# Kernel tuning notes

Hardware: AMD Instinct MI355X
Metric: run time of the kernel (lower is better)

Reference implementation:

```python
import jax, jax.numpy as jnp
import numpy as np

STEPS = 8  # number of scaling-and-squaring steps


def _identity_grid(D, H, W, dtype):
    # (D, H, W, 3) voxel-coordinate identity transformation
    z = jnp.arange(D, dtype=dtype)
    y = jnp.arange(H, dtype=dtype)
    x = jnp.arange(W, dtype=dtype)
    return jnp.stack(jnp.meshgrid(z, y, x, indexing='ij'), axis=-1)


def _pull_wrap(v, phi):
    """Trilinear sampling of field v at voxel coords phi with circular ('dft') bound.

    v:   (B, D, H, W, 3) vector field (values)
    phi: (B, D, H, W, 3) sampling coordinates in voxel space (z, y, x order)
    """
    B, D, H, W, C = v.shape
    f = jnp.floor(phi)
    w1 = phi - f          # weight of the +1 corner
    w0 = 1.0 - w1
    i0 = f.astype(jnp.int32)
    dims = jnp.array([D, H, W], dtype=jnp.int32)
    i0 = jnp.mod(i0, dims)          # wrap (dft) boundary
    i1 = jnp.mod(i0 + 1, dims)
    zs, ys, xs = (i0[..., 0], i1[..., 0]), (i0[..., 1], i1[..., 1]), (i0[..., 2], i1[..., 2])
    wzs, wys, wxs = (w0[..., 0], w1[..., 0]), (w0[..., 1], w1[..., 1]), (w0[..., 2], w1[..., 2])
    vflat = v.reshape(B, D * H * W, C)
    out = jnp.zeros_like(v)
    for a in range(2):
        for b in range(2):
            for c in range(2):
                lin = (zs[a] * H + ys[b]) * W + xs[c]              # (B, D, H, W)
                vals = jnp.take_along_axis(vflat, lin.reshape(B, -1, 1), axis=1)
                vals = vals.reshape(B, D, H, W, C)
                out = out + (wzs[a] * wys[b] * wxs[c])[..., None] * vals
    return out


def setup_inputs() -> dict:
    key = jax.random.key(0)
    velocity = jax.random.normal(key, (2, 128, 128, 128, 3), dtype=jnp.float32)
    return {"velocity": velocity}


def reference(velocity):
    # Scaling and squaring: v <- v/2^K; repeat K times: v <- v + v o (id + v)
    B, D, H, W, C = velocity.shape
    grid = _identity_grid(D, H, W, velocity.dtype)[None]  # (1, D, H, W, 3)
    v = velocity / (2.0 ** STEPS)
    for _ in range(STEPS):
        v = v + _pull_wrap(v, grid + v)
    # displacement=False -> return transformation field id + displacement
    return grid + v
```

## Files before the change

### kernel.cpp

```cpp
#include <hip/hip_runtime.h>
#include <hip/hip_fp16.h>


#define DHW   (128 * 128 * 128)
#define NVOX  (2 * DHW)
#define RW    129

__device__ __forceinline__ __half2 bc_h2(unsigned u) {
    return *reinterpret_cast<__half2*>(&u);
}

__device__ __forceinline__ void acc_cell(uint2 c, float w,
                                         float& az, float& ay, float& ax) {
    __half2 c0 = bc_h2(c.x), c1 = bc_h2(c.y);
    az = fmaf(w, __low2float(c0),  az);
    ay = fmaf(w, __high2float(c0), ay);
    ax = fmaf(w, __low2float(c1),  ax);
}

template <bool IN_F32, int H, int BX, int BZ>
__global__ __launch_bounds__(512) void sq_stencil(
    const float* __restrict__ vel,
    const uint2* __restrict__ fin,
    uint2* __restrict__ fout)
{
    constexpr int LBX = (BX == 64) ? 6 : 5;
    constexpr int LBZ = (BZ == 8) ? 3 : 2;
    constexpr int TX = BX + 2 * H, TY = 8 + 2 * H, TZ = BZ + 2 * H;
    constexpr int TS = TX * TY * TZ;
    constexpr int ZT  = 512 >> (LBX + 3);
    constexpr int VPT = BZ / ZT;
    constexpr int NXB = 128 / BX, LNX = 7 - LBX;
    constexpr int NZB = 128 / BZ, LNZ = 7 - LBZ;
    static_assert(TS * 8 <= 64 * 1024, "tile exceeds 64KB static LDS");
    static_assert(VPT == 4, "geometry expects 4 voxels/thread");
    __shared__ uint2 tile[TS];

    int t = (int)threadIdx.x;
    int b = (int)blockIdx.x;
    int X = (b & (NXB - 1)) << LBX;
    int b2 = b >> LNX;
    int Y = (b2 & 15) << 3;
    int b3 = b2 >> 4;
    int Z = (b3 & (NZB - 1)) << LBZ;
    int batch = b3 >> LNZ;
    int bbr = batch << 14;

    for (int idx = t; idx < TS; idx += 512) {
        int xx = idx % TX;
        int rem = idx / TX;
        int yy = rem % TY;
        int zz = rem / TY;
        int gx = (X - H + xx) & 127;
        int gy = (Y - H + yy) & 127;
        int gz = (Z - H + zz) & 127;
        uint2 c;
        if (IN_F32) {
            const float s = 1.0f / 256.0f;
            size_t a = (size_t)((batch << 21) | (gz << 14) | (gy << 7) | gx) * 3;
            __half2 p0 = __floats2half2_rn(vel[a] * s, vel[a + 1] * s);
            __half2 p1 = __floats2half2_rn(vel[a + 2] * s, 0.0f);
            c.x = *reinterpret_cast<unsigned*>(&p0);
            c.y = *reinterpret_cast<unsigned*>(&p1);
        } else {
            int rr = bbr + (gz << 7) + gy;
            c = fin[(rr << 7) + rr + gx];
        }
        tile[idx] = c;
    }
    __syncthreads();

    int lx = t & (BX - 1);
    int ly = (t >> LBX) & 7;
    int lz0 = (t >> (LBX + 3)) * VPT;

#pragma unroll
    for (int i = 0; i < VPT; ++i) {
        int lz = lz0 + i;
        int cidx = ((lz + H) * TY + (ly + H)) * TX + (lx + H);
        uint2 c = tile[cidx];
        __half2 c0 = bc_h2(c.x), c1 = bc_h2(c.y);
        float vz = __low2float(c0), vy = __high2float(c0), vx = __low2float(c1);

        float zf = (float)(Z + lz), yf = (float)(Y + ly), xf = (float)(X + lx);
        float pz = zf + vz, py = yf + vy, px = xf + vx;
        float fz = floorf(pz), fy = floorf(py), fx = floorf(px);
        float wz1 = pz - fz, wy1 = py - fy, wx1 = px - fx;
        float wz0 = 1.0f - wz1, wy0 = 1.0f - wy1, wx0 = 1.0f - wx1;

        int izl = (int)fz - Z + H;
        int iyl = (int)fy - Y + H;
        int ixl = (int)fx - X + H;

        float wzy00 = wz0 * wy0, wzy01 = wz0 * wy1;
        float wzy10 = wz1 * wy0, wzy11 = wz1 * wy1;

        float az = 0.0f, ay = 0.0f, ax = 0.0f;
        int i00 = (izl * TY + iyl) * TX + ixl;
        int i01 = i00 + TX;
        int i10 = i00 + TY * TX;
        int i11 = i10 + TX;

        acc_cell(tile[i00],     wzy00 * wx0, az, ay, ax);
        acc_cell(tile[i00 + 1], wzy00 * wx1, az, ay, ax);
        acc_cell(tile[i01],     wzy01 * wx0, az, ay, ax);
        acc_cell(tile[i01 + 1], wzy01 * wx1, az, ay, ax);
        acc_cell(tile[i10],     wzy10 * wx0, az, ay, ax);
        acc_cell(tile[i10 + 1], wzy10 * wx1, az, ay, ax);
        acc_cell(tile[i11],     wzy11 * wx0, az, ay, ax);
        acc_cell(tile[i11 + 1], wzy11 * wx1, az, ay, ax);

        float oz = vz + az, oy = vy + ay, ox = vx + ax;

        __half2 p0 = __floats2half2_rn(oz, oy);
        __half2 p1 = __floats2half2_rn(ox, 0.0f);
        uint2 sd;
        sd.x = *reinterpret_cast<unsigned*>(&p0);
        sd.y = *reinterpret_cast<unsigned*>(&p1);
        int z_ = Z + lz, y_ = Y + ly, x_ = X + lx;
        int rS = bbr + (z_ << 7) + y_;
        int pidx = (rS << 7) + rS + x_;
        fout[pidx] = sd;
        if (x_ == 0) fout[pidx + 128] = sd;
    }
}

__device__ __forceinline__ void acc_pair(uint4 g, float wl, float wr,
                                         float& az, float& ay, float& ax) {
    __half2 h0 = bc_h2(g.x);
    __half2 h1 = bc_h2(g.y);
    __half2 h2 = bc_h2(g.z);
    __half2 h3 = bc_h2(g.w);
    az += wl * __low2float(h0)  + wr * __low2float(h2);
    ay += wl * __high2float(h0) + wr * __high2float(h2);
    ax += wl * __low2float(h1)  + wr * __low2float(h3);
}

template <bool IN_F32, bool OUT_F32>
__global__ __launch_bounds__(1024) void sq_step_p(
    const void* __restrict__ vin_, void* __restrict__ vout_)
{
    const float* vinf = (const float*)vin_;
    const uint2* vinh = (const uint2*)vin_;

    int t = (int)threadIdx.x;
    int b = (int)blockIdx.x;
    int x = ((b & 1) << 6) | (t & 63);
    int y = (((b >> 1) & 31) << 2) | ((t >> 6) & 3);
    int z = (((b >> 6) & 31) << 2) | (t >> 8);
    int batch = b >> 11;

    const float s = IN_F32 ? (1.0f / 256.0f) : 1.0f;

    int bbr = batch << 14;
    int r   = bbr + (z << 7) + y;

    float vz, vy, vx;
    if (IN_F32) {
        size_t base = ((size_t)(batch << 21) + (z << 14) + (y << 7) + x) * 3;
        vz = vinf[base + 0] * s;
        vy = vinf[base + 1] * s;
        vx = vinf[base + 2] * s;
    } else {
        uint2 c = vinh[(r << 7) + r + x];
        __half2 c0 = bc_h2(c.x), c1 = bc_h2(c.y);
        vz = __low2float(c0); vy = __high2float(c0); vx = __low2float(c1);
    }

    float pz = (float)z + vz, py = (float)y + vy, px = (float)x + vx;
    float fz = floorf(pz), fy = floorf(py), fx = floorf(px);
    float wz1 = pz - fz, wy1 = py - fy, wx1 = px - fx;
    float wz0 = 1.0f - wz1, wy0 = 1.0f - wy1, wx0 = 1.0f - wx1;

    int iz0 = ((int)fz) & 127, iy0 = ((int)fy) & 127, ix0 = ((int)fx) & 127;
    int iz1 = (iz0 + 1) & 127, iy1 = (iy0 + 1) & 127;

    float wzy00 = wz0 * wy0, wzy01 = wz0 * wy1;
    float wzy10 = wz1 * wy0, wzy11 = wz1 * wy1;

    float az = 0.0f, ay = 0.0f, ax = 0.0f;

    if (IN_F32) {
        int bb  = batch << 21;
        int ix1 = (ix0 + 1) & 127;
        int zo0 = bb + (iz0 << 14), zo1 = bb + (iz1 << 14);
        int yo0 = iy0 << 7, yo1 = iy1 << 7;
#define CORNER(ZO, YO, IX, WW)                                          \
        {                                                               \
            size_t a = (size_t)((ZO) + (YO) + (IX)) * 3;                \
            float w = (WW);                                             \
            az += w * (vinf[a] * s);                                    \
            ay += w * (vinf[a + 1] * s);                                \
            ax += w * (vinf[a + 2] * s);                                \
        }
        CORNER(zo0, yo0, ix0, wzy00 * wx0)
        CORNER(zo0, yo0, ix1, wzy00 * wx1)
        CORNER(zo0, yo1, ix0, wzy01 * wx0)
        CORNER(zo0, yo1, ix1, wzy01 * wx1)
        CORNER(zo1, yo0, ix0, wzy10 * wx0)
        CORNER(zo1, yo0, ix1, wzy10 * wx1)
        CORNER(zo1, yo1, ix0, wzy11 * wx0)
        CORNER(zo1, yo1, ix1, wzy11 * wx1)
#undef CORNER
    } else {
        int r00 = bbr + (iz0 << 7) + iy0;
        int r01 = bbr + (iz0 << 7) + iy1;
        int r10 = bbr + (iz1 << 7) + iy0;
        int r11 = bbr + (iz1 << 7) + iy1;
        uint4 g00 = *(const uint4*)(vinh + (r00 << 7) + r00 + ix0);
        uint4 g01 = *(const uint4*)(vinh + (r01 << 7) + r01 + ix0);
        uint4 g10 = *(const uint4*)(vinh + (r10 << 7) + r10 + ix0);
        uint4 g11 = *(const uint4*)(vinh + (r11 << 7) + r11 + ix0);
        acc_pair(g00, wzy00 * wx0, wzy00 * wx1, az, ay, ax);
        acc_pair(g01, wzy01 * wx0, wzy01 * wx1, az, ay, ax);
        acc_pair(g10, wzy10 * wx0, wzy10 * wx1, az, ay, ax);
        acc_pair(g11, wzy11 * wx0, wzy11 * wx1, az, ay, ax);
    }

    float oz = vz + az;
    float oy = vy + ay;
    float ox = vx + ax;

    if (OUT_F32) {
        float* voutf = (float*)vout_;
        size_t base = ((size_t)(batch << 21) + (z << 14) + (y << 7) + x) * 3;
        voutf[base + 0] = oz + (float)z;
        voutf[base + 1] = oy + (float)y;
        voutf[base + 2] = ox + (float)x;
    } else {
        __half2 p0 = __floats2half2_rn(oz, oy);
        __half2 p1 = __floats2half2_rn(ox, 0.0f);
        uint2 sd;
        sd.x = *reinterpret_cast<unsigned*>(&p0);
        sd.y = *reinterpret_cast<unsigned*>(&p1);
        uint2* vouth = (uint2*)vout_;
        int pidx = (r << 7) + r + x;
        vouth[pidx] = sd;
        if (x == 0) vouth[pidx + 128] = sd;
    }
}

extern "C" void kernel_launch(void* const* d_in, const int* in_sizes, int n_in,
                              void* d_out, int out_size, void* d_ws, size_t ws_size,
                              hipStream_t stream) {
    const float* vel = (const float*)d_in[0];
    float* out = (float*)d_out;

    const size_t PB = (size_t)2 * 128 * 128 * RW * 8;

    dim3 sblock(512);
    dim3 sgrid(2048);
    dim3 ggrid(NVOX / 1024), gblock(1024);

    if (ws_size >= 2 * PB) {
        uint2* P0 = (uint2*)d_ws;
        uint2* P1 = (uint2*)((char*)d_ws + PB);

        sq_stencil<true,  1, 64, 4><<<sgrid, sblock, 0, stream>>>(vel, nullptr, P0);
        sq_stencil<false, 1, 64, 4><<<sgrid, sblock, 0, stream>>>(nullptr, P0, P1);
        sq_stencil<false, 1, 64, 4><<<sgrid, sblock, 0, stream>>>(nullptr, P1, P0);
        sq_stencil<false, 1, 64, 4><<<sgrid, sblock, 0, stream>>>(nullptr, P0, P1);
        sq_stencil<false, 1, 64, 4><<<sgrid, sblock, 0, stream>>>(nullptr, P1, P0);
        sq_stencil<false, 1, 64, 4><<<sgrid, sblock, 0, stream>>>(nullptr, P0, P1);
        sq_stencil<false, 2, 32, 8><<<sgrid, sblock, 0, stream>>>(nullptr, P1, P0);
        sq_step_p<false, true ><<<ggrid, gblock, 0, stream>>>(P0, out);
    } else {
        void* ws = d_ws;
        sq_step_p<true,  false><<<ggrid, gblock, 0, stream>>>(vel, ws);
        sq_step_p<false, false><<<ggrid, gblock, 0, stream>>>(ws,  out);
        sq_step_p<false, false><<<ggrid, gblock, 0, stream>>>(out, ws);
        sq_step_p<false, false><<<ggrid, gblock, 0, stream>>>(ws,  out);
        sq_step_p<false, false><<<ggrid, gblock, 0, stream>>>(out, ws);
        sq_step_p<false, false><<<ggrid, gblock, 0, stream>>>(ws,  out);
        sq_step_p<false, false><<<ggrid, gblock, 0, stream>>>(out, ws);
        sq_step_p<false, true ><<<ggrid, gblock, 0, stream>>>(ws,  out);
    }
}
```

Before: 280.7 us.

## Pipeline stencil steps over z-slabs with double-buffered LDS and separate f32 conversion

Each stencil block now walks four consecutive z-slabs, prefetching the next slab's halo into registers while computing the current one, then writing it into a second LDS buffer. The fp32-to-fp16 scaling moves into a dedicated vectorized conversion kernel, and intermediate steps use an unpadded layout, with only the last stencil writing the padded layout for the final gather kernel. This aims to hide global load latency and cut redundant halo traffic, at the cost of fewer blocks, more registers, one extra launch and a larger workspace requirement.

```diff
diff --git a/kernel.cpp b/kernel.cpp
--- a/kernel.cpp
+++ b/kernel.cpp
@@ -18,23 +18,40 @@
     ax = fmaf(w, __low2float(c1),  ax);
 }
 
-template <bool IN_F32, int H, int BX, int BZ>
-__global__ __launch_bounds__(512) void sq_stencil(
-    const float* __restrict__ vel,
-    const uint2* __restrict__ fin,
-    uint2* __restrict__ fout)
+__global__ __launch_bounds__(512) void conv_f32_f16(
+    const float* __restrict__ vel, uint2* __restrict__ out)
+{
+    int i = (((int)blockIdx.x << 9) | (int)threadIdx.x) << 1;
+    size_t a = (size_t)i * 3;
+    const float s = 1.0f / 256.0f;
+    float2 l0 = *(const float2*)(vel + a);
+    float2 l1 = *(const float2*)(vel + a + 2);
+    float2 l2 = *(const float2*)(vel + a + 4);
+    __half2 a0 = __floats2half2_rn(l0.x * s, l0.y * s);
+    __half2 a1 = __floats2half2_rn(l1.x * s, 0.0f);
+    __half2 b0 = __floats2half2_rn(l1.y * s, l2.x * s);
+    __half2 b1 = __floats2half2_rn(l2.y * s, 0.0f);
+    uint4 o;
+    o.x = *reinterpret_cast<unsigned*>(&a0);
+    o.y = *reinterpret_cast<unsigned*>(&a1);
+    o.z = *reinterpret_cast<unsigned*>(&b0);
+    o.w = *reinterpret_cast<unsigned*>(&b1);
+    *(uint4*)(out + i) = o;
+}
+
+template <int H, int BX, int BZ, int NB, bool PAD_OUT>
+__global__ __launch_bounds__(512) void sq_sten_pipe(
+    const uint2* __restrict__ fin, uint2* __restrict__ fout)
 {
     constexpr int LBX = (BX == 64) ? 6 : 5;
-    constexpr int LBZ = (BZ == 8) ? 3 : 2;
     constexpr int TX = BX + 2 * H, TY = 8 + 2 * H, TZ = BZ + 2 * H;
     constexpr int TS = TX * TY * TZ;
-    constexpr int ZT  = 512 >> (LBX + 3);
-    constexpr int VPT = BZ / ZT;
+    constexpr int PF = (TS + 511) / 512;
+    constexpr int VPT = (BX * BZ) / 64;
     constexpr int NXB = 128 / BX, LNX = 7 - LBX;
-    constexpr int NZB = 128 / BZ, LNZ = 7 - LBZ;
-    static_assert(TS * 8 <= 64 * 1024, "tile exceeds 64KB static LDS");
-    static_assert(VPT == 4, "geometry expects 4 voxels/thread");
-    __shared__ uint2 tile[TS];
+    static_assert(2 * TS * 8 <= 64 * 1024, "dbuf exceeds 64KB static LDS");
+    static_assert(128 % (BZ * NB) == 0 && 128 / (BZ * NB) == 8, "z grouping");
+    __shared__ uint2 lds[2][TS];
 
     int t = (int)threadIdx.x;
     int b = (int)blockIdx.x;
@@ -42,87 +59,119 @@
     int b2 = b >> LNX;
     int Y = (b2 & 15) << 3;
     int b3 = b2 >> 4;
-    int Z = (b3 & (NZB - 1)) << LBZ;
-    int batch = b3 >> LNZ;
-    int bbr = batch << 14;
-
-    for (int idx = t; idx < TS; idx += 512) {
-        int xx = idx % TX;
-        int rem = idx / TX;
-        int yy = rem % TY;
-        int zz = rem / TY;
-        int gx = (X - H + xx) & 127;
-        int gy = (Y - H + yy) & 127;
-        int gz = (Z - H + zz) & 127;
-        uint2 c;
-        if (IN_F32) {
-            const float s = 1.0f / 256.0f;
-            size_t a = (size_t)((batch << 21) | (gz << 14) | (gy << 7) | gx) * 3;
-            __half2 p0 = __floats2half2_rn(vel[a] * s, vel[a + 1] * s);
-            __half2 p1 = __floats2half2_rn(vel[a + 2] * s, 0.0f);
-            c.x = *reinterpret_cast<unsigned*>(&p0);
-            c.y = *reinterpret_cast<unsigned*>(&p1);
-        } else {
-            int rr = bbr + (gz << 7) + gy;
-            c = fin[(rr << 7) + rr + gx];
+    int Z0 = (b3 & 7) * (BZ * NB);
+    int batch = b3 >> 3;
+    int bb21 = batch << 21;
+
+    int soff[PF], szz[PF];
+#pragma unroll
+    for (int p = 0; p < PF; ++p) {
+        int idx = t + p * 512;
+        if (idx < TS) {
+            int xx = idx % TX;
+            int rem = idx / TX;
+            int yy = rem % TY;
+            int zz = rem / TY;
+            int gx = (X - H + xx) & 127;
+            int gy = (Y - H + yy) & 127;
+            soff[p] = (gy << 7) | gx;
+            szz[p] = zz;
         }
-        tile[idx] = c;
-    }
+    }
+
+    uint2 R[PF];
+#define STAGE_LOAD(ZB)                                                  \
+    _Pragma("unroll")                                                   \
+    for (int p = 0; p < PF; ++p) {                                      \
+        int idx = t + p * 512;                                          \
+        if (idx < TS) {                                                 \
+            int gz = ((ZB) - H + szz[p]) & 127;                         \
+            R[p] = fin[bb21 + (gz << 14) + soff[p]];                    \
+        }                                                               \
+    }
+#define DS_WRITE(BUF)                                                   \
+    _Pragma("unroll")                                                   \
+    for (int p = 0; p < PF; ++p) {                                      \
+        int idx = t + p * 512;                                          \
+        if (idx < TS) (BUF)[idx] = R[p];                                \
+    }
+
+    STAGE_LOAD(Z0)
+    DS_WRITE(lds[0])
     __syncthreads();
 
     int lx = t & (BX - 1);
     int ly = (t >> LBX) & 7;
     int lz0 = (t >> (LBX + 3)) * VPT;
 
+    for (int i = 0; i < NB; ++i) {
+        int Z = Z0 + i * BZ;
+        const uint2* tile = lds[i & 1];
+        if (i + 1 < NB) { STAGE_LOAD(Z0 + (i + 1) * BZ) }
+
+        uint2 sd[VPT];
 #pragma unroll
-    for (int i = 0; i < VPT; ++i) {
-        int lz = lz0 + i;
-        int cidx = ((lz + H) * TY + (ly + H)) * TX + (lx + H);
-        uint2 c = tile[cidx];
-        __half2 c0 = bc_h2(c.x), c1 = bc_h2(c.y);
-        float vz = __low2float(c0), vy = __high2float(c0), vx = __low2float(c1);
-
-        float zf = (float)(Z + lz), yf = (float)(Y + ly), xf = (float)(X + lx);
-        float pz = zf + vz, py = yf + vy, px = xf + vx;
-        float fz = floorf(pz), fy = floorf(py), fx = floorf(px);
-        float wz1 = pz - fz, wy1 = py - fy, wx1 = px - fx;
-        float wz0 = 1.0f - wz1, wy0 = 1.0f - wy1, wx0 = 1.0f - wx1;
-
-        int izl = (int)fz - Z + H;
-        int iyl = (int)fy - Y + H;
-        int ixl = (int)fx - X + H;
-
-        float wzy00 = wz0 * wy0, wzy01 = wz0 * wy1;
-        float wzy10 = wz1 * wy0, wzy11 = wz1 * wy1;
-
-        float az = 0.0f, ay = 0.0f, ax = 0.0f;
-        int i00 = (izl * TY + iyl) * TX + ixl;
-        int i01 = i00 + TX;
-        int i10 = i00 + TY * TX;
-        int i11 = i10 + TX;
-
-        acc_cell(tile[i00],     wzy00 * wx0, az, ay, ax);
-        acc_cell(tile[i00 + 1], wzy00 * wx1, az, ay, ax);
-        acc_cell(tile[i01],     wzy01 * wx0, az, ay, ax);
-        acc_cell(tile[i01 + 1], wzy01 * wx1, az, ay, ax);
-        acc_cell(tile[i10],     wzy10 * wx0, az, ay, ax);
-        acc_cell(tile[i10 + 1], wzy10 * wx1, az, ay, ax);
-        acc_cell(tile[i11],     wzy11 * wx0, az, ay, ax);
-        acc_cell(tile[i11 + 1], wzy11 * wx1, az, ay, ax);
-
-        float oz = vz + az, oy = vy + ay, ox = vx + ax;
-
-        __half2 p0 = __floats2half2_rn(oz, oy);
-        __half2 p1 = __floats2half2_rn(ox, 0.0f);
-        uint2 sd;
-        sd.x = *reinterpret_cast<unsigned*>(&p0);
-        sd.y = *reinterpret_cast<unsigned*>(&p1);
-        int z_ = Z + lz, y_ = Y + ly, x_ = X + lx;
-        int rS = bbr + (z_ << 7) + y_;
-        int pidx = (rS << 7) + rS + x_;
-        fout[pidx] = sd;
-        if (x_ == 0) fout[pidx + 128] = sd;
-    }
+        for (int v = 0; v < VPT; ++v) {
+            int lz = lz0 + v;
+            int cidx = ((lz + H) * TY + (ly + H)) * TX + (lx + H);
+            uint2 c = tile[cidx];
+            __half2 c0 = bc_h2(c.x), c1 = bc_h2(c.y);
+            float vz = __low2float(c0), vy = __high2float(c0), vx = __low2float(c1);
+
+            float pz = (float)(Z + lz) + vz;
+            float py = (float)(Y + ly) + vy;
+            float px = (float)(X + lx) + vx;
+            float fz = floorf(pz), fy = floorf(py), fx = floorf(px);
+            float wz1 = pz - fz, wy1 = py - fy, wx1 = px - fx;
+            float wz0 = 1.0f - wz1, wy0 = 1.0f - wy1, wx0 = 1.0f - wx1;
+
+            int izl = (int)fz - Z + H;
+            int iyl = (int)fy - Y + H;
+            int ixl = (int)fx - X + H;
+
+            float wzy00 = wz0 * wy0, wzy01 = wz0 * wy1;
+            float wzy10 = wz1 * wy0, wzy11 = wz1 * wy1;
+
+            float az = 0.0f, ay = 0.0f, ax = 0.0f;
+            int i00 = (izl * TY + iyl) * TX + ixl;
+            int i01 = i00 + TX;
+            int i10 = i00 + TY * TX;
+            int i11 = i10 + TX;
+
+            acc_cell(tile[i00],     wzy00 * wx0, az, ay, ax);
+            acc_cell(tile[i00 + 1], wzy00 * wx1, az, ay, ax);
+            acc_cell(tile[i01],     wzy01 * wx0, az, ay, ax);
+            acc_cell(tile[i01 + 1], wzy01 * wx1, az, ay, ax);
+            acc_cell(tile[i10],     wzy10 * wx0, az, ay, ax);
+            acc_cell(tile[i10 + 1], wzy10 * wx1, az, ay, ax);
+            acc_cell(tile[i11],     wzy11 * wx0, az, ay, ax);
+            acc_cell(tile[i11 + 1], wzy11 * wx1, az, ay, ax);
+
+            __half2 p0 = __floats2half2_rn(vz + az, vy + ay);
+            __half2 p1 = __floats2half2_rn(vx + ax, 0.0f);
+            sd[v].x = *reinterpret_cast<unsigned*>(&p0);
+            sd[v].y = *reinterpret_cast<unsigned*>(&p1);
+        }
+
+        if (i + 1 < NB) { DS_WRITE(lds[(i + 1) & 1]) }
+
+#pragma unroll
+        for (int v = 0; v < VPT; ++v) {
+            int lz = lz0 + v;
+            int z_ = Z + lz, y_ = Y + ly, x_ = X + lx;
+            if (PAD_OUT) {
+                int rS = (batch << 14) + (z_ << 7) + y_;
+                int pidx = (rS << 7) + rS + x_;
+                fout[pidx] = sd[v];
+                if (x_ == 0) fout[pidx + 128] = sd[v];
+            } else {
+                fout[bb21 | (z_ << 14) | (y_ << 7) | x_] = sd[v];
+            }
+        }
+        __syncthreads();
+    }
+#undef STAGE_LOAD
+#undef DS_WRITE
 }
 
 __device__ __forceinline__ void acc_pair(uint4 g, float wl, float wr,
@@ -246,24 +295,28 @@
     const float* vel = (const float*)d_in[0];
     float* out = (float*)d_out;
 
+    const size_t UB = (size_t)NVOX * 8;
     const size_t PB = (size_t)2 * 128 * 128 * RW * 8;
 
-    dim3 sblock(512);
-    dim3 sgrid(2048);
+    dim3 cgrid(NVOX / 1024), cblock(512);
+    dim3 pgrid1(512),  pblock(512);
+    dim3 pgrid2(1024);
     dim3 ggrid(NVOX / 1024), gblock(1024);
 
-    if (ws_size >= 2 * PB) {
-        uint2* P0 = (uint2*)d_ws;
-        uint2* P1 = (uint2*)((char*)d_ws + PB);
-
-        sq_stencil<true,  1, 64, 4><<<sgrid, sblock, 0, stream>>>(vel, nullptr, P0);
-        sq_stencil<false, 1, 64, 4><<<sgrid, sblock, 0, stream>>>(nullptr, P0, P1);
-        sq_stencil<false, 1, 64, 4><<<sgrid, sblock, 0, stream>>>(nullptr, P1, P0);
-        sq_stencil<false, 1, 64, 4><<<sgrid, sblock, 0, stream>>>(nullptr, P0, P1);
-        sq_stencil<false, 1, 64, 4><<<sgrid, sblock, 0, stream>>>(nullptr, P1, P0);
-        sq_stencil<false, 1, 64, 4><<<sgrid, sblock, 0, stream>>>(nullptr, P0, P1);
-        sq_stencil<false, 2, 32, 8><<<sgrid, sblock, 0, stream>>>(nullptr, P1, P0);
-        sq_step_p<false, true ><<<ggrid, gblock, 0, stream>>>(P0, out);
+    if (ws_size >= 2 * UB + PB) {
+        uint2* U0 = (uint2*)d_ws;
+        uint2* U1 = (uint2*)((char*)d_ws + UB);
+        uint2* P  = (uint2*)((char*)d_ws + 2 * UB);
+
+        conv_f32_f16<<<cgrid, cblock, 0, stream>>>(vel, U0);
+        sq_sten_pipe<1, 64, 4, 4, false><<<pgrid1, pblock, 0, stream>>>(U0, U1);
+        sq_sten_pipe<1, 64, 4, 4, false><<<pgrid1, pblock, 0, stream>>>(U1, U0);
+        sq_sten_pipe<1, 64, 4, 4, false><<<pgrid1, pblock, 0, stream>>>(U0, U1);
+        sq_sten_pipe<1, 64, 4, 4, false><<<pgrid1, pblock, 0, stream>>>(U1, U0);
+        sq_sten_pipe<1, 64, 4, 4, false><<<pgrid1, pblock, 0, stream>>>(U0, U1);
+        sq_sten_pipe<1, 64, 4, 4, false><<<pgrid1, pblock, 0, stream>>>(U1, U0);
+        sq_sten_pipe<2, 32, 4, 4, true ><<<pgrid2, pblock, 0, stream>>>(U0, P);
+        sq_step_p<false, true ><<<ggrid, gblock, 0, stream>>>(P, out);
     } else {
         void* ws = d_ws;
         sq_step_p<true,  false><<<ggrid, gblock, 0, stream>>>(vel, ws);
```

After: 295.4 us. +5.3%, slower.

## Warp-specialize stencil kernel with double-buffered LDS tiles across z-slabs

Applied to the files above, without the earlier changes.

Each stencil block now processes a 16-deep z range as four 4-slab chunks. Half the threads stage the next halo tile into a second LDS buffer while the other half compute the current chunk. Intermediate fields move to an unpadded layout, and only the last stencil writes the padded layout used by the final gather kernel. This aims to hide global load latency behind compute and cut redundant halo reloads. The cost is that only 256 threads compute per phase, LDS use doubles, and the grid is smaller, which lowers occupancy and parallelism.

```diff
diff --git a/kernel.cpp b/kernel.cpp
--- a/kernel.cpp
+++ b/kernel.cpp
@@ -18,23 +18,65 @@
     ax = fmaf(w, __low2float(c1),  ax);
 }
 
-template <bool IN_F32, int H, int BX, int BZ>
-__global__ __launch_bounds__(512) void sq_stencil(
-    const float* __restrict__ vel,
+template <int TXt, int TYt>
+__device__ __forceinline__ uint2 step_point(const uint2* __restrict__ tile,
+                                            uint2 c, int gz, int gy, int gx,
+                                            int OZ, int OY, int OX)
+{
+    __half2 c0 = bc_h2(c.x), c1 = bc_h2(c.y);
+    float vz = __low2float(c0), vy = __high2float(c0), vx = __low2float(c1);
+
+    float pz = (float)gz + vz, py = (float)gy + vy, px = (float)gx + vx;
+    float fz = floorf(pz), fy = floorf(py), fx = floorf(px);
+    float wz1 = pz - fz, wy1 = py - fy, wx1 = px - fx;
+    float wz0 = 1.0f - wz1, wy0 = 1.0f - wy1, wx0 = 1.0f - wx1;
+
+    int izl = (int)fz - OZ;
+    int iyl = (int)fy - OY;
+    int ixl = (int)fx - OX;
+
+    float wzy00 = wz0 * wy0, wzy01 = wz0 * wy1;
+    float wzy10 = wz1 * wy0, wzy11 = wz1 * wy1;
+
+    float az = 0.0f, ay = 0.0f, ax = 0.0f;
+    int i00 = (izl * TYt + iyl) * TXt + ixl;
+    int i01 = i00 + TXt;
+    int i10 = i00 + TYt * TXt;
+    int i11 = i10 + TXt;
+
+    acc_cell(tile[i00],     wzy00 * wx0, az, ay, ax);
+    acc_cell(tile[i00 + 1], wzy00 * wx1, az, ay, ax);
+    acc_cell(tile[i01],     wzy01 * wx0, az, ay, ax);
+    acc_cell(tile[i01 + 1], wzy01 * wx1, az, ay, ax);
+    acc_cell(tile[i10],     wzy10 * wx0, az, ay, ax);
+    acc_cell(tile[i10 + 1], wzy10 * wx1, az, ay, ax);
+    acc_cell(tile[i11],     wzy11 * wx0, az, ay, ax);
+    acc_cell(tile[i11 + 1], wzy11 * wx1, az, ay, ax);
+
+    __half2 p0 = __floats2half2_rn(vz + az, vy + ay);
+    __half2 p1 = __floats2half2_rn(vx + ax, 0.0f);
+    uint2 sd;
+    sd.x = *reinterpret_cast<unsigned*>(&p0);
+    sd.y = *reinterpret_cast<unsigned*>(&p1);
+    return sd;
+}
+
+template <bool IN_F32, int H, int BX, bool PAD_OUT>
+__global__ __launch_bounds__(512) void sq_sten_ws(
+    const float* __restrict__ velf,
     const uint2* __restrict__ fin,
     uint2* __restrict__ fout)
 {
     constexpr int LBX = (BX == 64) ? 6 : 5;
-    constexpr int LBZ = (BZ == 8) ? 3 : 2;
+    constexpr int BZ = 4, NB = 4;
     constexpr int TX = BX + 2 * H, TY = 8 + 2 * H, TZ = BZ + 2 * H;
     constexpr int TS = TX * TY * TZ;
-    constexpr int ZT  = 512 >> (LBX + 3);
-    constexpr int VPT = BZ / ZT;
     constexpr int NXB = 128 / BX, LNX = 7 - LBX;
-    constexpr int NZB = 128 / BZ, LNZ = 7 - LBZ;
-    static_assert(TS * 8 <= 64 * 1024, "tile exceeds 64KB static LDS");
-    static_assert(VPT == 4, "geometry expects 4 voxels/thread");
-    __shared__ uint2 tile[TS];
+    constexpr int YP = 256 / BX;
+    constexpr int YR = 8 / YP;
+    static_assert(2 * TS * 8 <= 64 * 1024, "dbuf exceeds 64KB static LDS");
+    __shared__ uint2 bufA[TS];
+    __shared__ uint2 bufB[TS];
 
     int t = (int)threadIdx.x;
     int b = (int)blockIdx.x;
@@ -42,87 +84,84 @@
     int b2 = b >> LNX;
     int Y = (b2 & 15) << 3;
     int b3 = b2 >> 4;
-    int Z = (b3 & (NZB - 1)) << LBZ;
-    int batch = b3 >> LNZ;
-    int bbr = batch << 14;
-
-    for (int idx = t; idx < TS; idx += 512) {
-        int xx = idx % TX;
-        int rem = idx / TX;
-        int yy = rem % TY;
-        int zz = rem / TY;
-        int gx = (X - H + xx) & 127;
-        int gy = (Y - H + yy) & 127;
-        int gz = (Z - H + zz) & 127;
-        uint2 c;
-        if (IN_F32) {
-            const float s = 1.0f / 256.0f;
-            size_t a = (size_t)((batch << 21) | (gz << 14) | (gy << 7) | gx) * 3;
-            __half2 p0 = __floats2half2_rn(vel[a] * s, vel[a + 1] * s);
-            __half2 p1 = __floats2half2_rn(vel[a + 2] * s, 0.0f);
-            c.x = *reinterpret_cast<unsigned*>(&p0);
-            c.y = *reinterpret_cast<unsigned*>(&p1);
-        } else {
-            int rr = bbr + (gz << 7) + gy;
-            c = fin[(rr << 7) + rr + gx];
-        }
-        tile[idx] = c;
-    }
+    int Z0 = (b3 & 7) << 4;
+    int batch = b3 >> 3;
+    int bb21 = batch << 21;
+
+#define STAGE_ONE(IDX, ZB, BUF)                                         \
+    {   int xx = (IDX) % TX;                                            \
+        int rem = (IDX) / TX;                                           \
+        int yy = rem % TY, zz = rem / TY;                               \
+        int gx = (X - H + xx) & 127;                                    \
+        int gy = (Y - H + yy) & 127;                                    \
+        int gz = ((ZB) - H + zz) & 127;                                 \
+        uint2 cc;                                                       \
+        if (IN_F32) {                                                   \
+            const float s = 1.0f / 256.0f;                              \
+            size_t a = (size_t)(bb21 | (gz << 14) | (gy << 7) | gx) * 3;\
+            __half2 q0 = __floats2half2_rn(velf[a] * s,                 \
+                                           velf[a + 1] * s);            \
+            __half2 q1 = __floats2half2_rn(velf[a + 2] * s, 0.0f);      \
+            cc.x = *reinterpret_cast<unsigned*>(&q0);                   \
+            cc.y = *reinterpret_cast<unsigned*>(&q1);                   \
+        } else {                                                        \
+            cc = fin[bb21 | (gz << 14) | (gy << 7) | gx];               \
+        }                                                               \
+        (BUF)[IDX] = cc;                                                \
+    }
+
+#define COMPUTE(TILE, Z)                                                \
+    {   int lx = t & (BX - 1);                                          \
+        int lyh = t >> LBX;                      \
+        _Pragma("unroll")                                               \
+        for (int j = 0; j < YR; ++j) {                                  \
+            int ly = lyh + j * YP;                                      \
+            _Pragma("unroll")                                           \
+            for (int lz = 0; lz < BZ; ++lz) {                           \
+                int ci = ((lz + H) * TY + (ly + H)) * TX + (lx + H);    \
+                uint2 sd = step_point<TX, TY>((TILE), (TILE)[ci],       \
+                                              (Z) + lz, Y + ly, X + lx, \
+                                              (Z) - H, Y - H, X - H);   \
+                int z_ = (Z) + lz, y_ = Y + ly, x_ = X + lx;            \
+                if (PAD_OUT) {                                          \
+                    int rS = (batch << 14) + (z_ << 7) + y_;            \
+                    int pidx = (rS << 7) + rS + x_;                     \
+                    fout[pidx] = sd;                                    \
+                    if (x_ == 0) fout[pidx + 128] = sd;                 \
+                } else {                                                \
+                    fout[bb21 | (z_ << 14) | (y_ << 7) | x_] = sd;      \
+                }                                                       \
+            }                                                           \
+        } }
+
+    for (int idx = t; idx < TS; idx += 512) STAGE_ONE(idx, Z0, bufA)
     __syncthreads();
 
-    int lx = t & (BX - 1);
-    int ly = (t >> LBX) & 7;
-    int lz0 = (t >> (LBX + 3)) * VPT;
-
-#pragma unroll
-    for (int i = 0; i < VPT; ++i) {
-        int lz = lz0 + i;
-        int cidx = ((lz + H) * TY + (ly + H)) * TX + (lx + H);
-        uint2 c = tile[cidx];
-        __half2 c0 = bc_h2(c.x), c1 = bc_h2(c.y);
-        float vz = __low2float(c0), vy = __high2float(c0), vx = __low2float(c1);
-
-        float zf = (float)(Z + lz), yf = (float)(Y + ly), xf = (float)(X + lx);
-        float pz = zf + vz, py = yf + vy, px = xf + vx;
-        float fz = floorf(pz), fy = floorf(py), fx = floorf(px);
-        float wz1 = pz - fz, wy1 = py - fy, wx1 = px - fx;
-        float wz0 = 1.0f - wz1, wy0 = 1.0f - wy1, wx0 = 1.0f - wx1;
-
-        int izl = (int)fz - Z + H;
-        int iyl = (int)fy - Y + H;
-        int ixl = (int)fx - X + H;
-
-        float wzy00 = wz0 * wy0, wzy01 = wz0 * wy1;
-        float wzy10 = wz1 * wy0, wzy11 = wz1 * wy1;
-
-        float az = 0.0f, ay = 0.0f, ax = 0.0f;
-        int i00 = (izl * TY + iyl) * TX + ixl;
-        int i01 = i00 + TX;
-        int i10 = i00 + TY * TX;
-        int i11 = i10 + TX;
-
-        acc_cell(tile[i00],     wzy00 * wx0, az, ay, ax);
-        acc_cell(tile[i00 + 1], wzy00 * wx1, az, ay, ax);
-        acc_cell(tile[i01],     wzy01 * wx0, az, ay, ax);
-        acc_cell(tile[i01 + 1], wzy01 * wx1, az, ay, ax);
-        acc_cell(tile[i10],     wzy10 * wx0, az, ay, ax);
-        acc_cell(tile[i10 + 1], wzy10 * wx1, az, ay, ax);
-        acc_cell(tile[i11],     wzy11 * wx0, az, ay, ax);
-        acc_cell(tile[i11 + 1], wzy11 * wx1, az, ay, ax);
-
-        float oz = vz + az, oy = vy + ay, ox = vx + ax;
-
-        __half2 p0 = __floats2half2_rn(oz, oy);
-        __half2 p1 = __floats2half2_rn(ox, 0.0f);
-        uint2 sd;
-        sd.x = *reinterpret_cast<unsigned*>(&p0);
-        sd.y = *reinterpret_cast<unsigned*>(&p1);
-        int z_ = Z + lz, y_ = Y + ly, x_ = X + lx;
-        int rS = bbr + (z_ << 7) + y_;
-        int pidx = (rS << 7) + rS + x_;
-        fout[pidx] = sd;
-        if (x_ == 0) fout[pidx + 128] = sd;
-    }
+    if (t >= 256) {
+        for (int idx = t - 256; idx < TS; idx += 256)
+            STAGE_ONE(idx, Z0 + BZ, bufB)
+    } else {
+        COMPUTE(bufA, Z0)
+    }
+    __syncthreads();
+    if (t >= 256) {
+        for (int idx = t - 256; idx < TS; idx += 256)
+            STAGE_ONE(idx, Z0 + 2 * BZ, bufA)
+    } else {
+        COMPUTE(bufB, Z0 + BZ)
+    }
+    __syncthreads();
+    if (t >= 256) {
+        for (int idx = t - 256; idx < TS; idx += 256)
+            STAGE_ONE(idx, Z0 + 3 * BZ, bufB)
+    } else {
+        COMPUTE(bufA, Z0 + 2 * BZ)
+    }
+    __syncthreads();
+    if (t < 256) COMPUTE(bufB, Z0 + 3 * BZ)
+
+#undef STAGE_ONE
+#undef COMPUTE
 }
 
 __device__ __forceinline__ void acc_pair(uint4 g, float wl, float wr,
@@ -246,24 +285,27 @@
     const float* vel = (const float*)d_in[0];
     float* out = (float*)d_out;
 
+    const size_t UB = (size_t)NVOX * 8;
     const size_t PB = (size_t)2 * 128 * 128 * RW * 8;
 
     dim3 sblock(512);
-    dim3 sgrid(2048);
+    dim3 sgrid1(512);
+    dim3 sgrid2(1024);
     dim3 ggrid(NVOX / 1024), gblock(1024);
 
-    if (ws_size >= 2 * PB) {
-        uint2* P0 = (uint2*)d_ws;
-        uint2* P1 = (uint2*)((char*)d_ws + PB);
-
-        sq_stencil<true,  1, 64, 4><<<sgrid, sblock, 0, stream>>>(vel, nullptr, P0);
-        sq_stencil<false, 1, 64, 4><<<sgrid, sblock, 0, stream>>>(nullptr, P0, P1);
-        sq_stencil<false, 1, 64, 4><<<sgrid, sblock, 0, stream>>>(nullptr, P1, P0);
-        sq_stencil<false, 1, 64, 4><<<sgrid, sblock, 0, stream>>>(nullptr, P0, P1);
-        sq_stencil<false, 1, 64, 4><<<sgrid, sblock, 0, stream>>>(nullptr, P1, P0);
-        sq_stencil<false, 1, 64, 4><<<sgrid, sblock, 0, stream>>>(nullptr, P0, P1);
-        sq_stencil<false, 2, 32, 8><<<sgrid, sblock, 0, stream>>>(nullptr, P1, P0);
-        sq_step_p<false, true ><<<ggrid, gblock, 0, stream>>>(P0, out);
+    if (ws_size >= 2 * UB + PB) {
+        uint2* U0 = (uint2*)d_ws;
+        uint2* U1 = (uint2*)((char*)d_ws + UB);
+        uint2* P  = (uint2*)((char*)d_ws + 2 * UB);
+
+        sq_sten_ws<true,  1, 64, false><<<sgrid1, sblock, 0, stream>>>(vel, nullptr, U0);
+        sq_sten_ws<false, 1, 64, false><<<sgrid1, sblock, 0, stream>>>(nullptr, U0, U1);
+        sq_sten_ws<false, 1, 64, false><<<sgrid1, sblock, 0, stream>>>(nullptr, U1, U0);
+        sq_sten_ws<false, 1, 64, false><<<sgrid1, sblock, 0, stream>>>(nullptr, U0, U1);
+        sq_sten_ws<false, 1, 64, false><<<sgrid1, sblock, 0, stream>>>(nullptr, U1, U0);
+        sq_sten_ws<false, 1, 64, false><<<sgrid1, sblock, 0, stream>>>(nullptr, U0, U1);
+        sq_sten_ws<false, 2, 32, true ><<<sgrid2, sblock, 0, stream>>>(nullptr, U1, P);
+        sq_step_p<false, true ><<<ggrid, gblock, 0, stream>>>(P, out);
     } else {
         void* ws = d_ws;
         sq_step_p<true,  false><<<ggrid, gblock, 0, stream>>>(vel, ws);
```

Measured after the change: 317.9 us. 13.3% more time.
